# Kernel tuning notes

Hardware: AMD Instinct MI355X
Metric: run time of the kernel (lower is better)

Reference implementation:

```python
import jax, jax.numpy as jnp
import numpy as np

ALPHA = 0.2          # LeakyReLU negative slope
MASK_VAL = -9e15     # matches torch -9000000000000000.0


def setup_inputs() -> dict:
    key = jax.random.key(0)
    k1, k2, k3, k4 = jax.random.split(key, 4)
    B, N, F_IN, F_OUT, DEG = 64, 1024, 64, 64, 8
    atoms = jax.random.normal(k1, (B, N, F_IN), dtype=jnp.float32)
    edges = jax.random.randint(k2, (B, N, DEG), 0, N, dtype=jnp.int64)
    # xavier_uniform with gain=1.414
    def xavier(k, shape, gain=1.414):
        fan_in, fan_out = shape[0], shape[1]
        bound = gain * np.sqrt(6.0 / (fan_in + fan_out))
        return jax.random.uniform(k, shape, jnp.float32, -bound, bound)
    W = xavier(k3, (F_IN, F_OUT))
    a = xavier(k4, (2 * F_OUT, 1))
    return {"atoms": atoms, "edges": edges, "W": W, "a": a}


def reference(atoms, edges, W, a):
    B, N, _ = atoms.shape
    F_OUT = W.shape[1]
    # h = atom @ W per graph -> [B, N, F_OUT]
    h = jnp.einsum('bnf,fo->bno', atoms, W)
    # Decompose concat-attention: e_ij = leakyrelu(h_i . a1 + h_j . a2)
    a1 = a[:F_OUT, 0]
    a2 = a[F_OUT:, 0]
    s1 = h @ a1  # [B, N]
    s2 = h @ a2  # [B, N]
    e = s1[:, :, None] + s2[:, None, :]  # [B, N, N]
    e = jnp.where(e > 0, e, ALPHA * e)   # LeakyReLU
    # Build adjacency mask from edge lists: adj[b, i, edges[b,i,d]] = True
    b_idx = jnp.arange(B)[:, None, None]
    i_idx = jnp.arange(N)[None, :, None]
    adj = jnp.zeros((B, N, N), dtype=bool).at[b_idx, i_idx, edges].set(True)
    e = jnp.where(adj, e, MASK_VAL)
    attn = jax.nn.softmax(e, axis=-1)    # [B, N, N]
    h_prime = jnp.einsum('bij,bjo->bio', attn, h)
    return jax.nn.elu(h_prime)
```

## Files before the change

### kernel.cpp

```cpp
#include <hip/hip_runtime.h>
#include <math.h>

#define BATCH 64
#define NNODE 1024
#define FDIM 64
#define DEG 8
#define ALPHA 0.2f
#define HSTR 66
#define WSTR 65

typedef __attribute__((ext_vector_type(8))) short bf16x8;
typedef __attribute__((ext_vector_type(4))) float f32x4;

__device__ __forceinline__ short f2bf(float f) {
    union { float f; unsigned u; } v; v.f = f;
    unsigned r = v.u + 0x7fffu + ((v.u >> 16) & 1u);
    return (short)(r >> 16);
}
__device__ __forceinline__ float bf2f(unsigned short s) {
    union { unsigned u; float f; } v; v.u = ((unsigned)s) << 16;
    return v.f;
}

__global__ __launch_bounds__(1024) void gat_fused(
    const float* __restrict__ atoms,
    const int*   __restrict__ edges,
    const float* __restrict__ W,
    const float* __restrict__ a,
    float* __restrict__ out)
{
    extern __shared__ char smem[];
    unsigned short* hl  = (unsigned short*)smem;
    float*          Wl  = (float*)(smem + NNODE * HSTR * 2);
    float*          s1l = Wl + FDIM * WSTR;
    float*          s2l = s1l + NNODE;
    float*          waL = s2l + NNODE;

    const int tid = threadIdx.x;
    const int bid = blockIdx.x;
    const int xcd = bid & 7, kk = bid >> 3;
    const int b     = xcd * 8 + (kk & 7);
    const int chunk = kk >> 3;

    #pragma unroll
    for (int i = 0; i < 4; ++i) {
        const int idx = tid + 1024 * i;
        Wl[(idx >> 6) * WSTR + (idx & 63)] = W[idx];
    }
    __syncthreads();

    const int lane = tid & 63;
    const int wvu  = __builtin_amdgcn_readfirstlane(tid >> 6);
    const int l16  = lane & 15;
    const int qd   = lane >> 4;

    if (tid < 2 * FDIM) {
        const int which = tid >> 6, kr = tid & 63;
        float p = 0.f;
        #pragma unroll
        for (int j = 0; j < FDIM; ++j)
            p = fmaf(Wl[kr * WSTR + j], a[which * FDIM + j], p);
        waL[which * FDIM + kr] = p;
    }

    bf16x8 Bw[2][4];
    #pragma unroll
    for (int ks = 0; ks < 2; ++ks)
        #pragma unroll
        for (int t = 0; t < 4; ++t)
            #pragma unroll
            for (int j = 0; j < 8; ++j)
                Bw[ks][t][j] = f2bf(Wl[(ks * 32 + qd * 8 + j) * WSTR + t * 16 + l16]);

    __syncthreads();

    bf16x8 Bs[2];
    #pragma unroll
    for (int ks = 0; ks < 2; ++ks)
        #pragma unroll
        for (int j = 0; j < 8; ++j) {
            const int k = ks * 32 + qd * 8 + j;
            const float v = (l16 == 0) ? waL[k] : ((l16 == 1) ? waL[FDIM + k] : 0.f);
            Bs[ks][j] = f2bf(v);
        }

    const float* __restrict__ ab = atoms + (size_t)b * NNODE * FDIM;
    #pragma unroll
    for (int t4 = 0; t4 < 4; ++t4) {
        const int rowbase = wvu * 64 + t4 * 16;
        const float* __restrict__ ar = ab + (size_t)(rowbase + l16) * FDIM;

        bf16x8 A[2];
        #pragma unroll
        for (int ks = 0; ks < 2; ++ks) {
            const float4 p0 = *(const float4*)(ar + ks * 32 + qd * 8);
            const float4 p1 = *(const float4*)(ar + ks * 32 + qd * 8 + 4);
            A[ks][0] = f2bf(p0.x); A[ks][1] = f2bf(p0.y);
            A[ks][2] = f2bf(p0.z); A[ks][3] = f2bf(p0.w);
            A[ks][4] = f2bf(p1.x); A[ks][5] = f2bf(p1.y);
            A[ks][6] = f2bf(p1.z); A[ks][7] = f2bf(p1.w);
        }

        f32x4 C[4] = {{0,0,0,0},{0,0,0,0},{0,0,0,0},{0,0,0,0}};
        f32x4 Cs = {0,0,0,0};
        #pragma unroll
        for (int ks = 0; ks < 2; ++ks) {
            #pragma unroll
            for (int t = 0; t < 4; ++t)
                C[t] = __builtin_amdgcn_mfma_f32_16x16x32_bf16(A[ks], Bw[ks][t], C[t], 0, 0, 0);
            Cs = __builtin_amdgcn_mfma_f32_16x16x32_bf16(A[ks], Bs[ks], Cs, 0, 0, 0);
        }

        #pragma unroll
        for (int t = 0; t < 4; ++t)
            #pragma unroll
            for (int r = 0; r < 4; ++r)
                hl[(rowbase + qd * 4 + r) * HSTR + t * 16 + l16] =
                    (unsigned short)f2bf(C[t][r]);

        if (l16 == 0) {
            #pragma unroll
            for (int r = 0; r < 4; ++r) s1l[rowbase + qd * 4 + r] = Cs[r];
        } else if (l16 == 1) {
            #pragma unroll
            for (int r = 0; r < 4; ++r) s2l[rowbase + qd * 4 + r] = Cs[r];
        }
    }
    __syncthreads();

    const int nodebase = chunk * 256 + wvu * 16;
    #pragma unroll 2
    for (int i = 0; i < 16; ++i) {
        const int node = nodebase + i;
        const int grow = b * NNODE + node;

        int ej[DEG];
        const int* __restrict__ ep = edges + (size_t)grow * DEG;
        #pragma unroll
        for (int k = 0; k < DEG; ++k) ej[k] = ep[k];

        const float si = s1l[node];
        float e[DEG], mx = -INFINITY;
        #pragma unroll
        for (int k = 0; k < DEG; ++k) {
            float v = si + s2l[ej[k]];
            v = (v > 0.f) ? v : ALPHA * v;
            e[k] = v; mx = fmaxf(mx, v);
        }
        float wgt[DEG], wsum = 0.f;
        #pragma unroll
        for (int k = 0; k < DEG; ++k) {
            bool kp = true;
            #pragma unroll
            for (int m = 0; m < DEG; ++m)
                if (m < k && ej[m] == ej[k]) kp = false;
            const float w = kp ? __expf(e[k] - mx) : 0.f;
            wgt[k] = w; wsum += w;
        }
        const float inv = 1.f / wsum;

        float acc = 0.f;
        #pragma unroll
        for (int k = 0; k < DEG; ++k)
            acc = fmaf(wgt[k] * inv, bf2f(hl[ej[k] * HSTR + lane]), acc);

        out[(size_t)grow * FDIM + lane] = (acc > 0.f) ? acc : (__expf(acc) - 1.f);
    }
}

extern "C" void kernel_launch(void* const* d_in, const int* in_sizes, int n_in,
                              void* d_out, int out_size, void* d_ws, size_t ws_size,
                              hipStream_t stream) {
    const float* atoms = (const float*)d_in[0];
    const int*   edges = (const int*)d_in[1];
    const float* W     = (const float*)d_in[2];
    const float* a     = (const float*)d_in[3];
    float* out = (float*)d_out;

    const size_t lds_bytes =
        (size_t)NNODE * HSTR * 2 +
        ((size_t)FDIM * WSTR + 2 * NNODE + 2 * FDIM) * 4;

    gat_fused<<<BATCH * 4, 1024, lds_bytes, stream>>>(atoms, edges, W, a, out);
}
```

Measured before the change: 103.7 us.

## Split fused GAT kernel into projection and aggregation kernels via global workspace

The single fused kernel recomputed h for a whole graph in each of 4 blocks per graph. It is replaced by two kernels. The first computes h (bf16), s1 and s2 once per row into the workspace using 1024 small blocks. The second gathers neighbour rows of h from global memory, with s2 and the edge list staged in LDS. This removes the 4x redundant projection and the large LDS footprint, which should raise occupancy. The cost is a global round trip for h and an extra kernel launch, and neighbour gathers now hit L2 instead of LDS.

```diff
diff --git a/kernel.cpp b/kernel.cpp
--- a/kernel.cpp
+++ b/kernel.cpp
@@ -6,7 +6,6 @@
 #define FDIM 64
 #define DEG 8
 #define ALPHA 0.2f
-#define HSTR 66
 #define WSTR 65
 
 typedef __attribute__((ext_vector_type(8))) short bf16x8;
@@ -22,35 +21,31 @@
     return v.f;
 }
 
-__global__ __launch_bounds__(1024) void gat_fused(
+__global__ __launch_bounds__(256) void gat_k1(
     const float* __restrict__ atoms,
-    const int*   __restrict__ edges,
     const float* __restrict__ W,
     const float* __restrict__ a,
-    float* __restrict__ out)
+    unsigned short* __restrict__ hg,
+    float* __restrict__ s1,
+    float* __restrict__ s2)
 {
-    extern __shared__ char smem[];
-    unsigned short* hl  = (unsigned short*)smem;
-    float*          Wl  = (float*)(smem + NNODE * HSTR * 2);
-    float*          s1l = Wl + FDIM * WSTR;
-    float*          s2l = s1l + NNODE;
-    float*          waL = s2l + NNODE;
+    __shared__ float Wl[FDIM * WSTR];
+    __shared__ float waL[2 * FDIM];
 
     const int tid = threadIdx.x;
     const int bid = blockIdx.x;
-    const int xcd = bid & 7, kk = bid >> 3;
-    const int b     = xcd * 8 + (kk & 7);
-    const int chunk = kk >> 3;
-
-    #pragma unroll
-    for (int i = 0; i < 4; ++i) {
-        const int idx = tid + 1024 * i;
+    const int b     = bid & 63;
+    const int chunk = bid >> 6;
+
+    #pragma unroll
+    for (int i = 0; i < 16; ++i) {
+        const int idx = tid + 256 * i;
         Wl[(idx >> 6) * WSTR + (idx & 63)] = W[idx];
     }
     __syncthreads();
 
     const int lane = tid & 63;
-    const int wvu  = __builtin_amdgcn_readfirstlane(tid >> 6);
+    const int wv   = __builtin_amdgcn_readfirstlane(tid >> 6);
     const int l16  = lane & 15;
     const int qd   = lane >> 4;
 
@@ -84,62 +79,80 @@
             Bs[ks][j] = f2bf(v);
         }
 
-    const float* __restrict__ ab = atoms + (size_t)b * NNODE * FDIM;
-    #pragma unroll
-    for (int t4 = 0; t4 < 4; ++t4) {
-        const int rowbase = wvu * 64 + t4 * 16;
-        const float* __restrict__ ar = ab + (size_t)(rowbase + l16) * FDIM;
-
-        bf16x8 A[2];
-        #pragma unroll
-        for (int ks = 0; ks < 2; ++ks) {
-            const float4 p0 = *(const float4*)(ar + ks * 32 + qd * 8);
-            const float4 p1 = *(const float4*)(ar + ks * 32 + qd * 8 + 4);
-            A[ks][0] = f2bf(p0.x); A[ks][1] = f2bf(p0.y);
-            A[ks][2] = f2bf(p0.z); A[ks][3] = f2bf(p0.w);
-            A[ks][4] = f2bf(p1.x); A[ks][5] = f2bf(p1.y);
-            A[ks][6] = f2bf(p1.z); A[ks][7] = f2bf(p1.w);
-        }
-
-        f32x4 C[4] = {{0,0,0,0},{0,0,0,0},{0,0,0,0},{0,0,0,0}};
-        f32x4 Cs = {0,0,0,0};
-        #pragma unroll
-        for (int ks = 0; ks < 2; ++ks) {
-            #pragma unroll
-            for (int t = 0; t < 4; ++t)
-                C[t] = __builtin_amdgcn_mfma_f32_16x16x32_bf16(A[ks], Bw[ks][t], C[t], 0, 0, 0);
-            Cs = __builtin_amdgcn_mfma_f32_16x16x32_bf16(A[ks], Bs[ks], Cs, 0, 0, 0);
-        }
-
+    const int grow0 = b * NNODE + chunk * 64 + wv * 16;
+    const float* __restrict__ ar = atoms + (size_t)(grow0 + l16) * FDIM;
+
+    bf16x8 A[2];
+    #pragma unroll
+    for (int ks = 0; ks < 2; ++ks) {
+        const float4 p0 = *(const float4*)(ar + ks * 32 + qd * 8);
+        const float4 p1 = *(const float4*)(ar + ks * 32 + qd * 8 + 4);
+        A[ks][0] = f2bf(p0.x); A[ks][1] = f2bf(p0.y);
+        A[ks][2] = f2bf(p0.z); A[ks][3] = f2bf(p0.w);
+        A[ks][4] = f2bf(p1.x); A[ks][5] = f2bf(p1.y);
+        A[ks][6] = f2bf(p1.z); A[ks][7] = f2bf(p1.w);
+    }
+
+    f32x4 C[4] = {{0,0,0,0},{0,0,0,0},{0,0,0,0},{0,0,0,0}};
+    f32x4 Cs = {0,0,0,0};
+    #pragma unroll
+    for (int ks = 0; ks < 2; ++ks) {
         #pragma unroll
         for (int t = 0; t < 4; ++t)
-            #pragma unroll
-            for (int r = 0; r < 4; ++r)
-                hl[(rowbase + qd * 4 + r) * HSTR + t * 16 + l16] =
-                    (unsigned short)f2bf(C[t][r]);
-
-        if (l16 == 0) {
-            #pragma unroll
-            for (int r = 0; r < 4; ++r) s1l[rowbase + qd * 4 + r] = Cs[r];
-        } else if (l16 == 1) {
-            #pragma unroll
-            for (int r = 0; r < 4; ++r) s2l[rowbase + qd * 4 + r] = Cs[r];
-        }
-    }
+            C[t] = __builtin_amdgcn_mfma_f32_16x16x32_bf16(A[ks], Bw[ks][t], C[t], 0, 0, 0);
+        Cs = __builtin_amdgcn_mfma_f32_16x16x32_bf16(A[ks], Bs[ks], Cs, 0, 0, 0);
+    }
+
+    #pragma unroll
+    for (int t = 0; t < 4; ++t)
+        #pragma unroll
+        for (int r = 0; r < 4; ++r)
+            hg[(size_t)(grow0 + qd * 4 + r) * FDIM + t * 16 + l16] =
+                (unsigned short)f2bf(C[t][r]);
+
+    if (l16 == 0) {
+        #pragma unroll
+        for (int r = 0; r < 4; ++r) s1[grow0 + qd * 4 + r] = Cs[r];
+    } else if (l16 == 1) {
+        #pragma unroll
+        for (int r = 0; r < 4; ++r) s2[grow0 + qd * 4 + r] = Cs[r];
+    }
+}
+
+__global__ __launch_bounds__(256) void gat_k2(
+    const unsigned short* __restrict__ hg,
+    const float* __restrict__ s1g,
+    const float* __restrict__ s2g,
+    const int*   __restrict__ edges,
+    float* __restrict__ out)
+{
+    __shared__ float s2l[NNODE];
+    __shared__ int   el[64 * DEG];
+    __shared__ float s1l[64];
+
+    const int tid = threadIdx.x;
+    const int bid = blockIdx.x;
+    const int b     = bid & 63;
+    const int chunk = bid >> 6;
+    const int rowbase = b * NNODE + chunk * 64;
+
+    ((float4*)s2l)[tid] = ((const float4*)(s2g + b * NNODE))[tid];
+    ((int2*)el)[tid]    = ((const int2*)(edges + (size_t)rowbase * DEG))[tid];
+    if (tid < 64) s1l[tid] = s1g[rowbase + tid];
     __syncthreads();
 
-    const int nodebase = chunk * 256 + wvu * 16;
+    const int lane = tid & 63;
+    const int wv   = tid >> 6;
+    const unsigned short* __restrict__ hb = hg + (size_t)b * NNODE * FDIM;
+
     #pragma unroll 2
     for (int i = 0; i < 16; ++i) {
-        const int node = nodebase + i;
-        const int grow = b * NNODE + node;
-
+        const int rl = wv * 16 + i;
         int ej[DEG];
-        const int* __restrict__ ep = edges + (size_t)grow * DEG;
-        #pragma unroll
-        for (int k = 0; k < DEG; ++k) ej[k] = ep[k];
-
-        const float si = s1l[node];
+        #pragma unroll
+        for (int k = 0; k < DEG; ++k) ej[k] = el[rl * DEG + k];
+
+        const float si = s1l[rl];
         float e[DEG], mx = -INFINITY;
         #pragma unroll
         for (int k = 0; k < DEG; ++k) {
@@ -162,9 +175,9 @@
         float acc = 0.f;
         #pragma unroll
         for (int k = 0; k < DEG; ++k)
-            acc = fmaf(wgt[k] * inv, bf2f(hl[ej[k] * HSTR + lane]), acc);
-
-        out[(size_t)grow * FDIM + lane] = (acc > 0.f) ? acc : (__expf(acc) - 1.f);
+            acc = fmaf(wgt[k] * inv, bf2f(hb[(size_t)ej[k] * FDIM + lane]), acc);
+
+        out[(size_t)(rowbase + rl) * FDIM + lane] = (acc > 0.f) ? acc : (__expf(acc) - 1.f);
     }
 }
 
@@ -177,9 +190,12 @@
     const float* a     = (const float*)d_in[3];
     float* out = (float*)d_out;
 
-    const size_t lds_bytes =
-        (size_t)NNODE * HSTR * 2 +
-        ((size_t)FDIM * WSTR + 2 * NNODE + 2 * FDIM) * 4;
-
-    gat_fused<<<BATCH * 4, 1024, lds_bytes, stream>>>(atoms, edges, W, a, out);
-}
+    const int rows = BATCH * NNODE;
+
+    unsigned short* hg = (unsigned short*)d_ws;
+    float* s1 = (float*)(hg + (size_t)rows * FDIM);
+    float* s2 = s1 + rows;
+
+    gat_k1<<<1024, 256, 0, stream>>>(atoms, W, a, hg, s1, s2);
+    gat_k2<<<1024, 256, 0, stream>>>(hg, s1, s2, edges, out);
+}
```

New measurement: 103.7 us. Within noise of the previous version (-0.0%).
